# Kernel tuning notes

Hardware: AMD Instinct MI355X
Metric: run time of the kernel (lower is better)

Reference implementation:

```python
import jax, jax.numpy as jnp
import numpy as np

MAX_S, MIN_S, MAX_R = 3.0, 0.5, 3.0
A = (MAX_S - MIN_S) / 2.0   # 1.25
B = (MAX_S + MIN_S) / 2.0   # 1.75
C = (MAX_R - 1.0) / 2.0     # 1.0
D = (MAX_R + 1.0) / 2.0     # 2.0

# 3x3 kernel base points, row-major: dim0 = dy, dim1 = dx, shape [2, 9]
BASE = jnp.array([[-1, -1], [-1, 0], [-1, 1], [0, -1], [0, 0], [0, 1],
                  [1, -1], [1, 0], [1, 1]], dtype=jnp.float32).T


def conv2d(x, w, b=None):
    y = jax.lax.conv_general_dilated(x, w, window_strides=(1, 1),
                                     padding=((1, 1), (1, 1)),
                                     dimension_numbers=('NCHW', 'OIHW', 'NCHW'))
    if b is not None:
        y = y + b[None, :, None, None]
    return y


def setup_inputs() -> dict:
    key = jax.random.key(0)
    ks = jax.random.split(key, 8)
    return {
        'x': jax.random.normal(ks[0], (8, 64, 128, 128), jnp.float32),
        'w_main': jax.random.normal(ks[1], (64, 64, 3, 3), jnp.float32) * 0.05,
        'w_rot': jax.random.normal(ks[2], (2, 64, 3, 3), jnp.float32) * 0.05,
        'b_rot': jax.random.normal(ks[3], (2,), jnp.float32) * 0.05,
        'w_str': jax.random.normal(ks[4], (1, 64, 3, 3), jnp.float32) * 0.05,
        'b_str': jax.random.normal(ks[5], (1,), jnp.float32) * 0.05,
        'w_whl': jax.random.normal(ks[6], (1, 64, 3, 3), jnp.float32) * 0.05,
        'b_whl': jax.random.normal(ks[7], (1,), jnp.float32) * 0.05,
    }


def reference(x, w_main, w_rot, b_rot, w_str, b_str, w_whl, b_whl):
    b, c, H, W = x.shape
    K = 9
    # --- offset generation ---
    rot = conv2d(x, w_rot, b_rot)                     # [b,2,H,W]
    sin, cos = rot[:, 0], rot[:, 1]
    norm = jnp.sqrt(sin ** 2 + cos ** 2 + 1e-6)
    sin, cos = sin / norm, cos / norm
    r = jnp.tanh(conv2d(x, w_str, b_str))[:, 0] * A + B   # [b,H,W]
    wr = jnp.tanh(conv2d(x, w_whl, b_whl))[:, 0] * C + D  # [b,H,W]
    ky, kx = BASE[0], BASE[1]                             # [9]
    kyb = ky[None, :, None, None]
    kxb = kx[None, :, None, None]
    o0 = kyb * (wr * r)[:, None]                          # [b,9,H,W]
    o1 = kxb * wr[:, None]
    sinb, cosb = sin[:, None], cos[:, None]
    dy = cosb * o0 + sinb * o1 - kyb                      # rotation then subtract base
    dx = -sinb * o0 + cosb * o1 - kxb
    # --- deformable sampling positions (stride=1, pad=1, dil=1) ---
    py = jnp.arange(H, dtype=x.dtype)[None, None, :, None] + kyb + dy  # [b,9,H,W]
    px = jnp.arange(W, dtype=x.dtype)[None, None, None, :] + kxb + dx
    y0f = jnp.floor(py); x0f = jnp.floor(px)
    ly = py - y0f; lx = px - x0f
    y0 = y0f.astype(jnp.int32); x0 = x0f.astype(jnp.int32)
    x_flat = x.reshape(b, c, H * W)

    def gather(yi, xi, wgt):
        valid = (yi >= 0) & (yi < H) & (xi >= 0) & (xi < W)
        idx = jnp.clip(yi, 0, H - 1) * W + jnp.clip(xi, 0, W - 1)
        g = jnp.take_along_axis(x_flat, idx.reshape(b, 1, -1), axis=2)
        g = g.reshape(b, c, K, H, W)
        return g * (wgt * valid)[:, None]

    val = (gather(y0, x0, (1 - ly) * (1 - lx))
           + gather(y0, x0 + 1, (1 - ly) * lx)
           + gather(y0 + 1, x0, ly * (1 - lx))
           + gather(y0 + 1, x0 + 1, ly * lx))          # [b,c,9,H,W]
    # final 3x3 conv over sampled points == contraction over (c, k)
    out = jnp.einsum('bckhw,ock->bohw', val, w_main.reshape(w_main.shape[0], c, K))
    return out
```

## Files before the change

### kernel.cpp

```cpp
#include <hip/hip_runtime.h>
#include <hip/hip_bf16.h>
#include <hip/hip_fp16.h>
#include <math.h>

#define HH 128
#define WW 128
#define HWSZ (HH*WW)
#define CH 64
#define OC 64
#define NB 8
#define RG 28
#define RPX (RG*RG)

#define XT_BYTES   (16777216u)
#define OFFS_BYTES (2097152u)

typedef _Float16 f16x8 __attribute__((ext_vector_type(8)));
typedef __attribute__((ext_vector_type(4))) float f32x4_t;

__global__ __launch_bounds__(256) void transpose_kernel(
    const float* __restrict__ x, const float* __restrict__ w_main,
    __half* __restrict__ xT, __half* __restrict__ wmT2)
{
    const int t = threadIdx.x;
    const int i = blockIdx.x;
    if (i >= 2048) {
        const int base = (i - 2048) * 4096 + t * 16;
        #pragma unroll
        for (int j = 0; j < 16; ++j) {
            const int e = base + j;
            const int k = e >> 12;
            const int r = e & 4095;
            const int o = r >> 6;
            const int c = r & 63;
            wmT2[e] = __float2half(w_main[(size_t)o * (CH * 9) + c * 9 + k]);
        }
        return;
    }
    __shared__ float tile[64][65];
    const int b = i & 7;
    const int j = i >> 3;
    const int h  = j >> 1;
    const int w0 = (j & 1) * 64;
    const float* xb = x + (size_t)b * CH * HWSZ + h * WW + w0;
    {
        const int w = t & 63, c0 = (t >> 6) * 16;
        #pragma unroll
        for (int jj = 0; jj < 16; ++jj)
            tile[c0 + jj][w] = xb[(size_t)(c0 + jj) * HWSZ + w];
    }
    __syncthreads();
    {
        const int c = t & 63, wq = t >> 6;
        __half* o = xT + ((size_t)b * HWSZ + h * WW + w0) * 64;
        #pragma unroll
        for (int jj = 0; jj < 16; ++jj) {
            const int w = wq * 16 + jj;
            o[(size_t)w * 64 + c] = __float2half(tile[c][w]);
        }
    }
}

__global__ __launch_bounds__(256) void offsets_kernel(
    const float* __restrict__ x,
    const float* __restrict__ w_rot,
    const float* __restrict__ w_str,
    const float* __restrict__ w_whl,
    float4* __restrict__ part)
{
    __shared__ float xs[8][4][WW];
    const int t  = threadIdx.x;
    const int i  = blockIdx.x;
    const int b  = i & 7;
    const int rp = (i >> 3) & 63;
    const int cg = i >> 9;
    const int h0 = rp * 2;
    const int c0 = cg * 8;
    const float* xb = x + (size_t)b * CH * HWSZ;
    #pragma unroll
    for (int jj = 0; jj < 4; ++jj) {
        const int u   = t + jj * 256;
        const int ch  = u >> 7;
        const int rem = u & 127;
        const int row = rem >> 5;
        const int w4  = (rem & 31) * 4;
        const int grow = h0 - 1 + row;
        float4 v = make_float4(0.f, 0.f, 0.f, 0.f);
        if (grow >= 0 && grow < HH)
            v = *(const float4*)&xb[((size_t)(c0 + ch) * HH + grow) * WW + w4];
        *(float4*)&xs[ch][row][w4] = v;
    }
    __syncthreads();
    const int r = t >> 7, w = t & 127;
    const int wl = max(w - 1, 0), wr2 = min(w + 1, WW - 1);
    const float ml = (w > 0) ? 1.f : 0.f, mr = (w < WW - 1) ? 1.f : 0.f;
    float a0 = 0.f, a1 = 0.f, a2 = 0.f, a3 = 0.f;
    #pragma unroll
    for (int ch = 0; ch < 8; ++ch) {
        const int cc = c0 + ch;
        #pragma unroll
        for (int dy = 0; dy < 3; ++dy) {
            const float* row_ = &xs[ch][r + dy][0];
            const float nl = row_[wl] * ml;
            const float nc = row_[w];
            const float nr = row_[wr2] * mr;
            const int d0 = cc * 9 + dy * 3;
            a0 = fmaf(nl, w_rot[d0 + 0], a0); a0 = fmaf(nc, w_rot[d0 + 1], a0); a0 = fmaf(nr, w_rot[d0 + 2], a0);
            a1 = fmaf(nl, w_rot[576 + d0 + 0], a1); a1 = fmaf(nc, w_rot[576 + d0 + 1], a1); a1 = fmaf(nr, w_rot[576 + d0 + 2], a1);
            a2 = fmaf(nl, w_str[d0 + 0], a2); a2 = fmaf(nc, w_str[d0 + 1], a2); a2 = fmaf(nr, w_str[d0 + 2], a2);
            a3 = fmaf(nl, w_whl[d0 + 0], a3); a3 = fmaf(nc, w_whl[d0 + 1], a3); a3 = fmaf(nr, w_whl[d0 + 2], a3);
        }
    }
    part[((size_t)cg * NB + b) * HWSZ + (h0 + r) * WW + w] = make_float4(a0, a1, a2, a3);
}

__global__ __launch_bounds__(256) void reduce_kernel(
    const float4* __restrict__ part,
    const float* __restrict__ b_rot, const float* __restrict__ b_str,
    const float* __restrict__ b_whl, float4* __restrict__ offs)
{
    const int i = blockIdx.x * 256 + threadIdx.x;
    float4 s = make_float4(0.f, 0.f, 0.f, 0.f);
    #pragma unroll
    for (int cg = 0; cg < 8; ++cg) {
        const float4 p = part[(size_t)cg * NB * HWSZ + i];
        s.x += p.x; s.y += p.y; s.z += p.z; s.w += p.w;
    }
    float sv = s.x + b_rot[0], cv = s.y + b_rot[1];
    const float inv = 1.0f / sqrtf(sv * sv + cv * cv + 1e-6f);
    const float rr = tanhf(s.z + b_str[0]) * 1.25f + 1.75f;
    const float wq = tanhf(s.w + b_whl[0]) * 1.0f + 2.0f;
    offs[i] = make_float4(sv * inv, cv * inv, wq * rr, wq);
}

__global__ __launch_bounds__(256, 3) void deform_kernel(
    const __half* __restrict__ xT, const __half* __restrict__ wmT2,
    const float4* __restrict__ offs, float* __restrict__ out)
{
    __shared__ union {
        uint4 xs[RPX * 4];
        float ots[64][67];
    } sh;
    const int t  = threadIdx.x;
    const int wv = t >> 6;
    const int l  = t & 63;
    const int lm = l & 15;
    const int lg = l >> 4;
    const int i  = blockIdx.x;
    const int b  = i & 7;
    const int tile = i >> 3;
    const int w0 = (tile & 15) * 8;
    const int h0 = (tile >> 4) * 8;
    const int pi = wv * 16 + lm;
    const int h = h0 + (pi >> 3);
    const int w = w0 + (pi & 7);
    const float4 o4 = offs[(size_t)b * HWSZ + h * WW + w];
    const float sv = o4.x, cv = o4.y, av = o4.z, wvl = o4.w;
    const float hh  = (float)h;
    const float wwf = (float)w;
    const __half* xb = xT + (size_t)b * HWSZ * 64;

    int ti[9], td[9];
    __half2 w2[9][4];
    #pragma unroll
    for (int k = 0; k < 9; ++k) {
        const float kyf = (float)(k / 3) - 1.f;
        const float kxf = (float)(k % 3) - 1.f;
        const float o0v = kyf * av;
        const float o1v = kxf * wvl;
        const float pyf = hh  + cv * o0v + sv * o1v;
        const float pxf = wwf - sv * o0v + cv * o1v;
        const float y0f = floorf(pyf), x0f = floorf(pxf);
        const float ly = pyf - y0f, lx = pxf - x0f;
        const int y0 = (int)y0f, x0i = (int)x0f;
        const int y1 = y0 + 1, x1 = x0i + 1;
        const bool vy0 = (y0 >= 0) && (y0 < HH);
        const bool vy1 = (y1 >= 0) && (y1 < HH);
        const bool vx0 = (x0i >= 0) && (x0i < WW);
        const bool vx1 = (x1 >= 0) && (x1 < WW);
        w2[k][0] = __float2half2_rn((1.f - ly) * (1.f - lx) * ((vy0 && vx0) ? 1.f : 0.f));
        w2[k][1] = __float2half2_rn((1.f - ly) * lx         * ((vy0 && vx1) ? 1.f : 0.f));
        w2[k][2] = __float2half2_rn(ly * (1.f - lx)         * ((vy1 && vx0) ? 1.f : 0.f));
        w2[k][3] = __float2half2_rn(ly * lx                 * ((vy1 && vx1) ? 1.f : 0.f));
        const int iy0 = min(max(y0, 0), HH - 1), iy1 = min(max(y1, 0), HH - 1);
        const int ix0 = min(max(x0i, 0), WW - 1), ix1 = min(max(x1, 0), WW - 1);
        ti[k] = (iy0 - (h0 - 10)) * RG + (ix0 - (w0 - 10));
        td[k] = (ix1 - ix0) | ((iy1 - iy0) << 1);
    }

    f32x4_t acc0 = {0.f, 0.f, 0.f, 0.f};
    f32x4_t acc1 = acc0, acc2 = acc0, acc3 = acc0;

    for (int g = 0; g < 2; ++g) {
        __syncthreads();
        for (int u = t; u < RPX * 4; u += 256) {
            const int pxu = u >> 2, q = u & 3;
            const int lr = pxu / RG;
            const int lc = pxu - lr * RG;
            const int gy = min(max(h0 - 10 + lr, 0), HH - 1);
            const int gx = min(max(w0 - 10 + lc, 0), WW - 1);
            sh.xs[pxu * 4 + (q ^ (pxu & 3))] =
                *(const uint4*)(xb + (size_t)(gy * WW + gx) * 64 + g * 32 + q * 8);
        }
        __syncthreads();
        const int cb0 = g * 32 + lg * 8;
        #pragma unroll
        for (int k = 0; k < 9; ++k) {
            const int i00 = ti[k];
            const int dxx = td[k] & 1;
            const int dyy = (td[k] >> 1) * RG;
            const int i01 = i00 + dxx;
            const int i10 = i00 + dyy;
            const int i11 = i10 + dxx;
            union Q { uint4 q; __half2 h2[4]; };
            Q q00, q01, q10, q11;
            q00.q = sh.xs[i00 * 4 + (lg ^ (i00 & 3))];
            q01.q = sh.xs[i01 * 4 + (lg ^ (i01 & 3))];
            q10.q = sh.xs[i10 * 4 + (lg ^ (i10 & 3))];
            q11.q = sh.xs[i11 * 4 + (lg ^ (i11 & 3))];
            union { __half2 h2[4]; f16x8 v; } af;
            #pragma unroll
            for (int j = 0; j < 4; ++j) {
                af.h2[j] = __hfma2(q00.h2[j], w2[k][0],
                           __hfma2(q01.h2[j], w2[k][1],
                           __hfma2(q10.h2[j], w2[k][2],
                           __hmul2(q11.h2[j], w2[k][3]))));
            }
            const __half* wp = wmT2 + ((size_t)k * 64 + lm) * 64 + cb0;
            const f16x8 bf0 = *(const f16x8*)(wp);
            const f16x8 bf1 = *(const f16x8*)(wp + 1024);
            const f16x8 bf2v = *(const f16x8*)(wp + 2048);
            const f16x8 bf3 = *(const f16x8*)(wp + 3072);
            acc0 = __builtin_amdgcn_mfma_f32_16x16x32_f16(af.v, bf0,  acc0, 0, 0, 0);
            acc1 = __builtin_amdgcn_mfma_f32_16x16x32_f16(af.v, bf1,  acc1, 0, 0, 0);
            acc2 = __builtin_amdgcn_mfma_f32_16x16x32_f16(af.v, bf2v, acc2, 0, 0, 0);
            acc3 = __builtin_amdgcn_mfma_f32_16x16x32_f16(af.v, bf3,  acc3, 0, 0, 0);
        }
    }
    __syncthreads();
    const int pxw = wv * 16 + lg * 4;
    #pragma unroll
    for (int rg2 = 0; rg2 < 4; ++rg2) {
        sh.ots[pxw + rg2][ 0 + lm] = acc0[rg2];
        sh.ots[pxw + rg2][16 + lm] = acc1[rg2];
        sh.ots[pxw + rg2][32 + lm] = acc2[rg2];
        sh.ots[pxw + rg2][48 + lm] = acc3[rg2];
    }
    __syncthreads();
    const int oo = t >> 2;
    const int q  = (t & 3) * 16;
    #pragma unroll
    for (int j2 = 0; j2 < 4; ++j2) {
        const int px = q + j2 * 4;
        float4 v = make_float4(sh.ots[px + 0][oo], sh.ots[px + 1][oo],
                               sh.ots[px + 2][oo], sh.ots[px + 3][oo]);
        *(float4*)&out[((size_t)b * OC + oo) * HWSZ +
                       (h0 + (px >> 3)) * WW + w0 + (px & 7)] = v;
    }
}

extern "C" void kernel_launch(void* const* d_in, const int* in_sizes, int n_in,
                              void* d_out, int out_size, void* d_ws, size_t ws_size,
                              hipStream_t stream)
{
    const float* x      = (const float*)d_in[0];
    const float* w_main = (const float*)d_in[1];
    const float* w_rot  = (const float*)d_in[2];
    const float* b_rot  = (const float*)d_in[3];
    const float* w_str  = (const float*)d_in[4];
    const float* b_str  = (const float*)d_in[5];
    const float* w_whl  = (const float*)d_in[6];
    const float* b_whl  = (const float*)d_in[7];
    float* out = (float*)d_out;

    char* ws = (char*)d_ws;
    __half*  xT   = (__half*)ws;
    float4*  offs = (float4*)(ws + XT_BYTES);
    __half*  wmT2 = (__half*)(ws + XT_BYTES + OFFS_BYTES);
    float4*  part = (float4*)d_out;

    transpose_kernel<<<dim3(2057), 256, 0, stream>>>(x, w_main, xT, wmT2);
    offsets_kernel<<<dim3(4096), 256, 0, stream>>>(x, w_rot, w_str, w_whl, part);
    reduce_kernel<<<dim3(NB * HWSZ / 256), 256, 0, stream>>>(
        part, b_rot, b_str, b_whl, offs);
    deform_kernel<<<dim3(2048), 256, 0, stream>>>(xT, wmT2, offs, out);
}
```

Baseline: 213.1 us.

## Enlarge deform tile to 16x8 and stage halo via direct global-to-LDS loads

Each deform_kernel block now covers a 16x8 pixel tile with 512 threads instead of 8x8 with 256, so the 36x28 halo region is shared by twice as many pixels. This cuts redundant staging traffic per output pixel. Staging uses global_load_lds, which writes straight into LDS and skips the register round trip, and the XOR swizzle is applied on the global-address side. The offset fetch and first stage are issued before the sampling-weight computation so the two overlap. The launch bound of (512,4) may tighten the register budget and cause spills, and the larger output staging buffer raises LDS use.

```diff
diff --git a/kernel.cpp b/kernel.cpp
--- a/kernel.cpp
+++ b/kernel.cpp
@@ -9,8 +9,14 @@
 #define CH 64
 #define OC 64
 #define NB 8
-#define RG 28
-#define RPX (RG*RG)
+
+#define TH 16
+#define TW 8
+#define RGR 36
+#define RGC 28
+#define RPX2 (RGR*RGC)
+#define NQ (RPX2*4)
+#define NCHUNK (NQ/64)
 
 #define XT_BYTES   (16777216u)
 #define OFFS_BYTES (2097152u)
@@ -133,13 +139,13 @@
     offs[i] = make_float4(sv * inv, cv * inv, wq * rr, wq);
 }
 
-__global__ __launch_bounds__(256, 3) void deform_kernel(
+__global__ __launch_bounds__(512, 4) void deform_kernel(
     const __half* __restrict__ xT, const __half* __restrict__ wmT2,
     const float4* __restrict__ offs, float* __restrict__ out)
 {
     __shared__ union {
-        uint4 xs[RPX * 4];
-        float ots[64][67];
+        uint4 xs[NQ];
+        float ots[128][67];
     } sh;
     const int t  = threadIdx.x;
     const int wv = t >> 6;
@@ -149,16 +155,38 @@
     const int i  = blockIdx.x;
     const int b  = i & 7;
     const int tile = i >> 3;
-    const int w0 = (tile & 15) * 8;
-    const int h0 = (tile >> 4) * 8;
+    const int w0 = (tile & 15) * TW;
+    const int h0 = (tile >> 4) * TH;
     const int pi = wv * 16 + lm;
     const int h = h0 + (pi >> 3);
     const int w = w0 + (pi & 7);
+    const __half* xb = xT + (size_t)b * HWSZ * 64;
+
     const float4 o4 = offs[(size_t)b * HWSZ + h * WW + w];
+
+    auto stage = [&](int g) {
+        for (int c = wv; c < NCHUNK; c += 8) {
+            const int u   = c * 64 + l;
+            const int pxu = u >> 2;
+            const int sq  = u & 3;
+            const int lr  = pxu / RGC;
+            const int lc  = pxu - lr * RGC;
+            const int gy  = min(max(h0 - 10 + lr, 0), HH - 1);
+            const int gx  = min(max(w0 - 10 + lc, 0), WW - 1);
+            const int sq2 = sq ^ (pxu & 3);
+            const __half* gp = xb + ((size_t)(gy * WW + gx) * 64 + g * 32 + sq2 * 8);
+            __builtin_amdgcn_global_load_lds(
+                (const __attribute__((address_space(1))) void*)gp,
+                (__attribute__((address_space(3))) void*)((char*)sh.xs + (size_t)c * 1024),
+                16, 0, 0);
+        }
+    };
+
+    stage(0);
+
     const float sv = o4.x, cv = o4.y, av = o4.z, wvl = o4.w;
     const float hh  = (float)h;
     const float wwf = (float)w;
-    const __half* xb = xT + (size_t)b * HWSZ * 64;
 
     int ti[9], td[9];
     __half2 w2[9][4];
@@ -184,31 +212,20 @@
         w2[k][3] = __float2half2_rn(ly * lx                 * ((vy1 && vx1) ? 1.f : 0.f));
         const int iy0 = min(max(y0, 0), HH - 1), iy1 = min(max(y1, 0), HH - 1);
         const int ix0 = min(max(x0i, 0), WW - 1), ix1 = min(max(x1, 0), WW - 1);
-        ti[k] = (iy0 - (h0 - 10)) * RG + (ix0 - (w0 - 10));
+        ti[k] = (iy0 - (h0 - 10)) * RGC + (ix0 - (w0 - 10));
         td[k] = (ix1 - ix0) | ((iy1 - iy0) << 1);
     }
 
     f32x4_t acc0 = {0.f, 0.f, 0.f, 0.f};
     f32x4_t acc1 = acc0, acc2 = acc0, acc3 = acc0;
 
-    for (int g = 0; g < 2; ++g) {
-        __syncthreads();
-        for (int u = t; u < RPX * 4; u += 256) {
-            const int pxu = u >> 2, q = u & 3;
-            const int lr = pxu / RG;
-            const int lc = pxu - lr * RG;
-            const int gy = min(max(h0 - 10 + lr, 0), HH - 1);
-            const int gx = min(max(w0 - 10 + lc, 0), WW - 1);
-            sh.xs[pxu * 4 + (q ^ (pxu & 3))] =
-                *(const uint4*)(xb + (size_t)(gy * WW + gx) * 64 + g * 32 + q * 8);
-        }
-        __syncthreads();
+    auto compute = [&](int g) {
         const int cb0 = g * 32 + lg * 8;
         #pragma unroll
         for (int k = 0; k < 9; ++k) {
             const int i00 = ti[k];
             const int dxx = td[k] & 1;
-            const int dyy = (td[k] >> 1) * RG;
+            const int dyy = (td[k] >> 1) * RGC;
             const int i01 = i00 + dxx;
             const int i10 = i00 + dyy;
             const int i11 = i10 + dxx;
@@ -236,7 +253,15 @@
             acc2 = __builtin_amdgcn_mfma_f32_16x16x32_f16(af.v, bf2v, acc2, 0, 0, 0);
             acc3 = __builtin_amdgcn_mfma_f32_16x16x32_f16(af.v, bf3,  acc3, 0, 0, 0);
         }
-    }
+    };
+
+    __syncthreads();
+    compute(0);
+    __syncthreads();
+    stage(1);
+    __syncthreads();
+    compute(1);
+
     __syncthreads();
     const int pxw = wv * 16 + lg * 4;
     #pragma unroll
@@ -247,15 +272,18 @@
         sh.ots[pxw + rg2][48 + lm] = acc3[rg2];
     }
     __syncthreads();
-    const int oo = t >> 2;
-    const int q  = (t & 3) * 16;
+    const int oo = t >> 3;
+    const int s  = t & 7;
     #pragma unroll
     for (int j2 = 0; j2 < 4; ++j2) {
-        const int px = q + j2 * 4;
-        float4 v = make_float4(sh.ots[px + 0][oo], sh.ots[px + 1][oo],
-                               sh.ots[px + 2][oo], sh.ots[px + 3][oo]);
+        const int idx  = s * 4 + j2;
+        const int r    = idx >> 1;
+        const int colh = idx & 1;
+        const int p0   = r * 8 + colh * 4;
+        float4 v = make_float4(sh.ots[p0 + 0][oo], sh.ots[p0 + 1][oo],
+                               sh.ots[p0 + 2][oo], sh.ots[p0 + 3][oo]);
         *(float4*)&out[((size_t)b * OC + oo) * HWSZ +
-                       (h0 + (px >> 3)) * WW + w0 + (px & 7)] = v;
+                       (h0 + r) * WW + w0 + colh * 4] = v;
     }
 }
 
@@ -283,5 +311,5 @@
     offsets_kernel<<<dim3(4096), 256, 0, stream>>>(x, w_rot, w_str, w_whl, part);
     reduce_kernel<<<dim3(NB * HWSZ / 256), 256, 0, stream>>>(
         part, b_rot, b_str, b_whl, offs);
-    deform_kernel<<<dim3(2048), 256, 0, stream>>>(xT, wmT2, offs, out);
-}
+    deform_kernel<<<dim3(1024), 512, 0, stream>>>(xT, wmT2, offs, out);
+}
```

Result: slower. 225.1 us (+5.6%).

## Gather deformable samples directly from global memory instead of staging LDS halo

Applied to the files above, without the earlier changes.

Removes the 28x28 LDS halo tile staged per channel half and gathers the four bilinear corner vectors straight from the fp16 channel-last input in global memory. Both channel halves are processed in one pass over the 9 taps, and occupancy is raised to 4 blocks per CU because LDS use drops to the output transpose buffer. This avoids loading a large halo (784 pixels for 64 outputs) and two barriers per half, in exchange for scattered 16-byte global loads that depend on L1/L2 hits. There is also a risk of extra load latency without LDS reuse.

```diff
diff --git a/kernel.cpp b/kernel.cpp
--- a/kernel.cpp
+++ b/kernel.cpp
@@ -9,8 +9,6 @@
 #define CH 64
 #define OC 64
 #define NB 8
-#define RG 28
-#define RPX (RG*RG)
 
 #define XT_BYTES   (16777216u)
 #define OFFS_BYTES (2097152u)
@@ -133,14 +131,11 @@
     offs[i] = make_float4(sv * inv, cv * inv, wq * rr, wq);
 }
 
-__global__ __launch_bounds__(256, 3) void deform_kernel(
+__global__ __launch_bounds__(256, 4) void deform_kernel(
     const __half* __restrict__ xT, const __half* __restrict__ wmT2,
     const float4* __restrict__ offs, float* __restrict__ out)
 {
-    __shared__ union {
-        uint4 xs[RPX * 4];
-        float ots[64][67];
-    } sh;
+    __shared__ float ots[64][67];
     const int t  = threadIdx.x;
     const int wv = t >> 6;
     const int l  = t & 63;
@@ -154,13 +149,14 @@
     const int pi = wv * 16 + lm;
     const int h = h0 + (pi >> 3);
     const int w = w0 + (pi & 7);
+    const __half* xb = xT + (size_t)b * HWSZ * 64;
+
     const float4 o4 = offs[(size_t)b * HWSZ + h * WW + w];
     const float sv = o4.x, cv = o4.y, av = o4.z, wvl = o4.w;
     const float hh  = (float)h;
     const float wwf = (float)w;
-    const __half* xb = xT + (size_t)b * HWSZ * 64;
-
-    int ti[9], td[9];
+
+    int ti_[9], td_[9];
     __half2 w2[9][4];
     #pragma unroll
     for (int k = 0; k < 9; ++k) {
@@ -184,67 +180,75 @@
         w2[k][3] = __float2half2_rn(ly * lx                 * ((vy1 && vx1) ? 1.f : 0.f));
         const int iy0 = min(max(y0, 0), HH - 1), iy1 = min(max(y1, 0), HH - 1);
         const int ix0 = min(max(x0i, 0), WW - 1), ix1 = min(max(x1, 0), WW - 1);
-        ti[k] = (iy0 - (h0 - 10)) * RG + (ix0 - (w0 - 10));
-        td[k] = (ix1 - ix0) | ((iy1 - iy0) << 1);
+        ti_[k] = iy0 * WW + ix0;
+        td_[k] = (ix1 - ix0) | ((iy1 - iy0) << 1);
     }
 
     f32x4_t acc0 = {0.f, 0.f, 0.f, 0.f};
     f32x4_t acc1 = acc0, acc2 = acc0, acc3 = acc0;
 
-    for (int g = 0; g < 2; ++g) {
-        __syncthreads();
-        for (int u = t; u < RPX * 4; u += 256) {
-            const int pxu = u >> 2, q = u & 3;
-            const int lr = pxu / RG;
-            const int lc = pxu - lr * RG;
-            const int gy = min(max(h0 - 10 + lr, 0), HH - 1);
-            const int gx = min(max(w0 - 10 + lc, 0), WW - 1);
-            sh.xs[pxu * 4 + (q ^ (pxu & 3))] =
-                *(const uint4*)(xb + (size_t)(gy * WW + gx) * 64 + g * 32 + q * 8);
-        }
-        __syncthreads();
-        const int cb0 = g * 32 + lg * 8;
-        #pragma unroll
-        for (int k = 0; k < 9; ++k) {
-            const int i00 = ti[k];
-            const int dxx = td[k] & 1;
-            const int dyy = (td[k] >> 1) * RG;
-            const int i01 = i00 + dxx;
-            const int i10 = i00 + dyy;
-            const int i11 = i10 + dxx;
-            union Q { uint4 q; __half2 h2[4]; };
-            Q q00, q01, q10, q11;
-            q00.q = sh.xs[i00 * 4 + (lg ^ (i00 & 3))];
-            q01.q = sh.xs[i01 * 4 + (lg ^ (i01 & 3))];
-            q10.q = sh.xs[i10 * 4 + (lg ^ (i10 & 3))];
-            q11.q = sh.xs[i11 * 4 + (lg ^ (i11 & 3))];
-            union { __half2 h2[4]; f16x8 v; } af;
-            #pragma unroll
-            for (int j = 0; j < 4; ++j) {
-                af.h2[j] = __hfma2(q00.h2[j], w2[k][0],
-                           __hfma2(q01.h2[j], w2[k][1],
-                           __hfma2(q10.h2[j], w2[k][2],
-                           __hmul2(q11.h2[j], w2[k][3]))));
-            }
-            const __half* wp = wmT2 + ((size_t)k * 64 + lm) * 64 + cb0;
-            const f16x8 bf0 = *(const f16x8*)(wp);
-            const f16x8 bf1 = *(const f16x8*)(wp + 1024);
-            const f16x8 bf2v = *(const f16x8*)(wp + 2048);
-            const f16x8 bf3 = *(const f16x8*)(wp + 3072);
-            acc0 = __builtin_amdgcn_mfma_f32_16x16x32_f16(af.v, bf0,  acc0, 0, 0, 0);
-            acc1 = __builtin_amdgcn_mfma_f32_16x16x32_f16(af.v, bf1,  acc1, 0, 0, 0);
-            acc2 = __builtin_amdgcn_mfma_f32_16x16x32_f16(af.v, bf2v, acc2, 0, 0, 0);
-            acc3 = __builtin_amdgcn_mfma_f32_16x16x32_f16(af.v, bf3,  acc3, 0, 0, 0);
-        }
-    }
-    __syncthreads();
+    union Q { uint4 q; __half2 h2[4]; };
+    union AF { __half2 h2[4]; f16x8 v; };
+
+    #pragma unroll
+    for (int k = 0; k < 9; ++k) {
+        const int i00 = ti_[k];
+        const int dxx = td_[k] & 1;
+        const int dyy = (td_[k] >> 1) * WW;
+        const int i01 = i00 + dxx;
+        const int i10 = i00 + dyy;
+        const int i11 = i10 + dxx;
+        const __half* p00 = xb + (size_t)i00 * 64 + lg * 8;
+        const __half* p01 = xb + (size_t)i01 * 64 + lg * 8;
+        const __half* p10 = xb + (size_t)i10 * 64 + lg * 8;
+        const __half* p11 = xb + (size_t)i11 * 64 + lg * 8;
+        Q a00, a01, a10, a11, c00, c01, c10, c11;
+        a00.q = *(const uint4*)(p00);
+        a01.q = *(const uint4*)(p01);
+        a10.q = *(const uint4*)(p10);
+        a11.q = *(const uint4*)(p11);
+        c00.q = *(const uint4*)(p00 + 32);
+        c01.q = *(const uint4*)(p01 + 32);
+        c10.q = *(const uint4*)(p10 + 32);
+        c11.q = *(const uint4*)(p11 + 32);
+        AF af0, af1;
+        #pragma unroll
+        for (int j = 0; j < 4; ++j) {
+            af0.h2[j] = __hfma2(a00.h2[j], w2[k][0],
+                        __hfma2(a01.h2[j], w2[k][1],
+                        __hfma2(a10.h2[j], w2[k][2],
+                        __hmul2(a11.h2[j], w2[k][3]))));
+            af1.h2[j] = __hfma2(c00.h2[j], w2[k][0],
+                        __hfma2(c01.h2[j], w2[k][1],
+                        __hfma2(c10.h2[j], w2[k][2],
+                        __hmul2(c11.h2[j], w2[k][3]))));
+        }
+        const __half* wp = wmT2 + ((size_t)k * 64 + lm) * 64 + lg * 8;
+        const f16x8 b00 = *(const f16x8*)(wp);
+        const f16x8 b01 = *(const f16x8*)(wp + 1024);
+        const f16x8 b02 = *(const f16x8*)(wp + 2048);
+        const f16x8 b03 = *(const f16x8*)(wp + 3072);
+        const f16x8 b10 = *(const f16x8*)(wp + 32);
+        const f16x8 b11 = *(const f16x8*)(wp + 1024 + 32);
+        const f16x8 b12 = *(const f16x8*)(wp + 2048 + 32);
+        const f16x8 b13 = *(const f16x8*)(wp + 3072 + 32);
+        acc0 = __builtin_amdgcn_mfma_f32_16x16x32_f16(af0.v, b00, acc0, 0, 0, 0);
+        acc1 = __builtin_amdgcn_mfma_f32_16x16x32_f16(af0.v, b01, acc1, 0, 0, 0);
+        acc2 = __builtin_amdgcn_mfma_f32_16x16x32_f16(af0.v, b02, acc2, 0, 0, 0);
+        acc3 = __builtin_amdgcn_mfma_f32_16x16x32_f16(af0.v, b03, acc3, 0, 0, 0);
+        acc0 = __builtin_amdgcn_mfma_f32_16x16x32_f16(af1.v, b10, acc0, 0, 0, 0);
+        acc1 = __builtin_amdgcn_mfma_f32_16x16x32_f16(af1.v, b11, acc1, 0, 0, 0);
+        acc2 = __builtin_amdgcn_mfma_f32_16x16x32_f16(af1.v, b12, acc2, 0, 0, 0);
+        acc3 = __builtin_amdgcn_mfma_f32_16x16x32_f16(af1.v, b13, acc3, 0, 0, 0);
+    }
+
     const int pxw = wv * 16 + lg * 4;
     #pragma unroll
     for (int rg2 = 0; rg2 < 4; ++rg2) {
-        sh.ots[pxw + rg2][ 0 + lm] = acc0[rg2];
-        sh.ots[pxw + rg2][16 + lm] = acc1[rg2];
-        sh.ots[pxw + rg2][32 + lm] = acc2[rg2];
-        sh.ots[pxw + rg2][48 + lm] = acc3[rg2];
+        ots[pxw + rg2][ 0 + lm] = acc0[rg2];
+        ots[pxw + rg2][16 + lm] = acc1[rg2];
+        ots[pxw + rg2][32 + lm] = acc2[rg2];
+        ots[pxw + rg2][48 + lm] = acc3[rg2];
     }
     __syncthreads();
     const int oo = t >> 2;
@@ -252,8 +256,8 @@
     #pragma unroll
     for (int j2 = 0; j2 < 4; ++j2) {
         const int px = q + j2 * 4;
-        float4 v = make_float4(sh.ots[px + 0][oo], sh.ots[px + 1][oo],
-                               sh.ots[px + 2][oo], sh.ots[px + 3][oo]);
+        float4 v = make_float4(ots[px + 0][oo], ots[px + 1][oo],
+                               ots[px + 2][oo], ots[px + 3][oo]);
         *(float4*)&out[((size_t)b * OC + oo) * HWSZ +
                        (h0 + (px >> 3)) * WW + w0 + (px & 7)] = v;
     }
```

New measurement: 252.4 us. 1.18x slower.

## Merge transpose and offset kernels; prefetch tiles and weights in deform kernel

Applied to the files above, without the earlier changes.

Fuses the transpose and offsets kernels into one launch so they can run concurrently on the GPU. In the deform kernel, the first channel-half tile is loaded into registers before the offset and bilinear index math, so global-load latency overlaps with that computation. The next tap's weight fragments are prefetched during the current tap's MFMAs, and shared-memory indices are precomputed with a changed swizzle. In exchange, the extra staged uint4 registers (13 of them) may reduce occupancy.

```diff
diff --git a/kernel.cpp b/kernel.cpp
--- a/kernel.cpp
+++ b/kernel.cpp
@@ -18,14 +18,19 @@
 typedef _Float16 f16x8 __attribute__((ext_vector_type(8)));
 typedef __attribute__((ext_vector_type(4))) float f32x4_t;
 
-__global__ __launch_bounds__(256) void transpose_kernel(
+__global__ __launch_bounds__(256) void pre_kernel(
     const float* __restrict__ x, const float* __restrict__ w_main,
-    __half* __restrict__ xT, __half* __restrict__ wmT2)
+    const float* __restrict__ w_rot, const float* __restrict__ w_str,
+    const float* __restrict__ w_whl,
+    __half* __restrict__ xT, __half* __restrict__ wmT2,
+    float4* __restrict__ part)
 {
+    __shared__ float shmem[64 * 65];
     const int t = threadIdx.x;
     const int i = blockIdx.x;
-    if (i >= 2048) {
-        const int base = (i - 2048) * 4096 + t * 16;
+
+    if (i >= 6144) {
+        const int base = (i - 6144) * 4096 + t * 16;
         #pragma unroll
         for (int j = 0; j < 16; ++j) {
             const int e = base + j;
@@ -37,40 +42,35 @@
         }
         return;
     }
-    __shared__ float tile[64][65];
-    const int b = i & 7;
-    const int j = i >> 3;
-    const int h  = j >> 1;
-    const int w0 = (j & 1) * 64;
-    const float* xb = x + (size_t)b * CH * HWSZ + h * WW + w0;
-    {
-        const int w = t & 63, c0 = (t >> 6) * 16;
-        #pragma unroll
-        for (int jj = 0; jj < 16; ++jj)
-            tile[c0 + jj][w] = xb[(size_t)(c0 + jj) * HWSZ + w];
-    }
-    __syncthreads();
-    {
-        const int c = t & 63, wq = t >> 6;
-        __half* o = xT + ((size_t)b * HWSZ + h * WW + w0) * 64;
-        #pragma unroll
-        for (int jj = 0; jj < 16; ++jj) {
-            const int w = wq * 16 + jj;
-            o[(size_t)w * 64 + c] = __float2half(tile[c][w]);
-        }
-    }
-}
-
-__global__ __launch_bounds__(256) void offsets_kernel(
-    const float* __restrict__ x,
-    const float* __restrict__ w_rot,
-    const float* __restrict__ w_str,
-    const float* __restrict__ w_whl,
-    float4* __restrict__ part)
-{
-    __shared__ float xs[8][4][WW];
-    const int t  = threadIdx.x;
-    const int i  = blockIdx.x;
+
+    if (i >= 4096) {
+        float (*tile)[65] = (float(*)[65])shmem;
+        const int it = i - 4096;
+        const int b = it & 7;
+        const int j = it >> 3;
+        const int h  = j >> 1;
+        const int w0 = (j & 1) * 64;
+        const float* xb = x + (size_t)b * CH * HWSZ + h * WW + w0;
+        {
+            const int w = t & 63, c0 = (t >> 6) * 16;
+            #pragma unroll
+            for (int jj = 0; jj < 16; ++jj)
+                tile[c0 + jj][w] = xb[(size_t)(c0 + jj) * HWSZ + w];
+        }
+        __syncthreads();
+        {
+            const int c = t & 63, wq = t >> 6;
+            __half* o = xT + ((size_t)b * HWSZ + h * WW + w0) * 64;
+            #pragma unroll
+            for (int jj = 0; jj < 16; ++jj) {
+                const int w = wq * 16 + jj;
+                o[(size_t)w * 64 + c] = __float2half(tile[c][w]);
+            }
+        }
+        return;
+    }
+
+    float (*xs)[4][WW] = (float(*)[4][WW])shmem;
     const int b  = i & 7;
     const int rp = (i >> 3) & 63;
     const int cg = i >> 9;
@@ -154,13 +154,28 @@
     const int pi = wv * 16 + lm;
     const int h = h0 + (pi >> 3);
     const int w = w0 + (pi & 7);
+    const __half* xb = xT + (size_t)b * HWSZ * 64;
+
+    uint4 st[13];
+    #pragma unroll
+    for (int j = 0; j < 13; ++j) {
+        const int u = t + j * 256;
+        if (u < RPX * 4) {
+            const int pxu = u >> 2, q = u & 3;
+            const int lr = pxu / RG;
+            const int lc = pxu - lr * RG;
+            const int gy = min(max(h0 - 10 + lr, 0), HH - 1);
+            const int gx = min(max(w0 - 10 + lc, 0), WW - 1);
+            st[j] = *(const uint4*)(xb + (size_t)(gy * WW + gx) * 64 + q * 8);
+        }
+    }
+
     const float4 o4 = offs[(size_t)b * HWSZ + h * WW + w];
     const float sv = o4.x, cv = o4.y, av = o4.z, wvl = o4.w;
     const float hh  = (float)h;
     const float wwf = (float)w;
-    const __half* xb = xT + (size_t)b * HWSZ * 64;
-
-    int ti[9], td[9];
+
+    int idx00[9], idx01[9], idx10[9], idx11[9];
     __half2 w2[9][4];
     #pragma unroll
     for (int k = 0; k < 9; ++k) {
@@ -184,59 +199,82 @@
         w2[k][3] = __float2half2_rn(ly * lx                 * ((vy1 && vx1) ? 1.f : 0.f));
         const int iy0 = min(max(y0, 0), HH - 1), iy1 = min(max(y1, 0), HH - 1);
         const int ix0 = min(max(x0i, 0), WW - 1), ix1 = min(max(x1, 0), WW - 1);
-        ti[k] = (iy0 - (h0 - 10)) * RG + (ix0 - (w0 - 10));
-        td[k] = (ix1 - ix0) | ((iy1 - iy0) << 1);
+        const int dyy = iy1 - iy0, dxx = ix1 - ix0;
+        const int p00 = (iy0 - (h0 - 10)) * RG + (ix0 - (w0 - 10));
+        const int p01 = p00 + dxx;
+        const int p10 = p00 + dyy * RG;
+        const int p11 = p10 + dxx;
+        idx00[k] = p00 * 4 + (lg ^ ((p00 >> 1) & 3));
+        idx01[k] = p01 * 4 + (lg ^ ((p01 >> 1) & 3));
+        idx10[k] = p10 * 4 + (lg ^ ((p10 >> 1) & 3));
+        idx11[k] = p11 * 4 + (lg ^ ((p11 >> 1) & 3));
+    }
+
+    #pragma unroll
+    for (int j = 0; j < 13; ++j) {
+        const int u = t + j * 256;
+        if (u < RPX * 4) {
+            const int pxu = u >> 2, q = u & 3;
+            sh.xs[pxu * 4 + (q ^ ((pxu >> 1) & 3))] = st[j];
+        }
     }
 
     f32x4_t acc0 = {0.f, 0.f, 0.f, 0.f};
     f32x4_t acc1 = acc0, acc2 = acc0, acc3 = acc0;
 
-    for (int g = 0; g < 2; ++g) {
-        __syncthreads();
-        for (int u = t; u < RPX * 4; u += 256) {
-            const int pxu = u >> 2, q = u & 3;
-            const int lr = pxu / RG;
-            const int lc = pxu - lr * RG;
-            const int gy = min(max(h0 - 10 + lr, 0), HH - 1);
-            const int gx = min(max(w0 - 10 + lc, 0), WW - 1);
-            sh.xs[pxu * 4 + (q ^ (pxu & 3))] =
-                *(const uint4*)(xb + (size_t)(gy * WW + gx) * 64 + g * 32 + q * 8);
-        }
-        __syncthreads();
+    auto compute = [&](int g) {
         const int cb0 = g * 32 + lg * 8;
+        const __half* wb = wmT2 + lm * 64 + cb0;
+        f16x8 bc0 = *(const f16x8*)(wb);
+        f16x8 bc1 = *(const f16x8*)(wb + 1024);
+        f16x8 bc2 = *(const f16x8*)(wb + 2048);
+        f16x8 bc3 = *(const f16x8*)(wb + 3072);
         #pragma unroll
         for (int k = 0; k < 9; ++k) {
-            const int i00 = ti[k];
-            const int dxx = td[k] & 1;
-            const int dyy = (td[k] >> 1) * RG;
-            const int i01 = i00 + dxx;
-            const int i10 = i00 + dyy;
-            const int i11 = i10 + dxx;
+            f16x8 bn0, bn1, bn2, bn3;
+            if (k < 8) {
+                const __half* wp = wb + (size_t)(k + 1) * 4096;
+                bn0 = *(const f16x8*)(wp);
+                bn1 = *(const f16x8*)(wp + 1024);
+                bn2 = *(const f16x8*)(wp + 2048);
+                bn3 = *(const f16x8*)(wp + 3072);
+            }
             union Q { uint4 q; __half2 h2[4]; };
             Q q00, q01, q10, q11;
-            q00.q = sh.xs[i00 * 4 + (lg ^ (i00 & 3))];
-            q01.q = sh.xs[i01 * 4 + (lg ^ (i01 & 3))];
-            q10.q = sh.xs[i10 * 4 + (lg ^ (i10 & 3))];
-            q11.q = sh.xs[i11 * 4 + (lg ^ (i11 & 3))];
+            q00.q = sh.xs[idx00[k]];
+            q01.q = sh.xs[idx01[k]];
+            q10.q = sh.xs[idx10[k]];
+            q11.q = sh.xs[idx11[k]];
             union { __half2 h2[4]; f16x8 v; } af;
             #pragma unroll
             for (int j = 0; j < 4; ++j) {
-                af.h2[j] = __hfma2(q00.h2[j], w2[k][0],
-                           __hfma2(q01.h2[j], w2[k][1],
-                           __hfma2(q10.h2[j], w2[k][2],
-                           __hmul2(q11.h2[j], w2[k][3]))));
+                const __half2 e0 = __hfma2(q00.h2[j], w2[k][0], __hmul2(q01.h2[j], w2[k][1]));
+                const __half2 e1 = __hfma2(q10.h2[j], w2[k][2], __hmul2(q11.h2[j], w2[k][3]));
+                af.h2[j] = __hadd2(e0, e1);
             }
-            const __half* wp = wmT2 + ((size_t)k * 64 + lm) * 64 + cb0;
-            const f16x8 bf0 = *(const f16x8*)(wp);
-            const f16x8 bf1 = *(const f16x8*)(wp + 1024);
-            const f16x8 bf2v = *(const f16x8*)(wp + 2048);
-            const f16x8 bf3 = *(const f16x8*)(wp + 3072);
-            acc0 = __builtin_amdgcn_mfma_f32_16x16x32_f16(af.v, bf0,  acc0, 0, 0, 0);
-            acc1 = __builtin_amdgcn_mfma_f32_16x16x32_f16(af.v, bf1,  acc1, 0, 0, 0);
-            acc2 = __builtin_amdgcn_mfma_f32_16x16x32_f16(af.v, bf2v, acc2, 0, 0, 0);
-            acc3 = __builtin_amdgcn_mfma_f32_16x16x32_f16(af.v, bf3,  acc3, 0, 0, 0);
-        }
-    }
+            acc0 = __builtin_amdgcn_mfma_f32_16x16x32_f16(af.v, bc0, acc0, 0, 0, 0);
+            acc1 = __builtin_amdgcn_mfma_f32_16x16x32_f16(af.v, bc1, acc1, 0, 0, 0);
+            acc2 = __builtin_amdgcn_mfma_f32_16x16x32_f16(af.v, bc2, acc2, 0, 0, 0);
+            acc3 = __builtin_amdgcn_mfma_f32_16x16x32_f16(af.v, bc3, acc3, 0, 0, 0);
+            if (k < 8) { bc0 = bn0; bc1 = bn1; bc2 = bn2; bc3 = bn3; }
+        }
+    };
+
+    __syncthreads();
+    compute(0);
+    __syncthreads();
+    for (int u = t; u < RPX * 4; u += 256) {
+        const int pxu = u >> 2, q = u & 3;
+        const int lr = pxu / RG;
+        const int lc = pxu - lr * RG;
+        const int gy = min(max(h0 - 10 + lr, 0), HH - 1);
+        const int gx = min(max(w0 - 10 + lc, 0), WW - 1);
+        sh.xs[pxu * 4 + (q ^ ((pxu >> 1) & 3))] =
+            *(const uint4*)(xb + (size_t)(gy * WW + gx) * 64 + 32 + q * 8);
+    }
+    __syncthreads();
+    compute(1);
+
     __syncthreads();
     const int pxw = wv * 16 + lg * 4;
     #pragma unroll
@@ -279,8 +317,8 @@
     __half*  wmT2 = (__half*)(ws + XT_BYTES + OFFS_BYTES);
     float4*  part = (float4*)d_out;
 
-    transpose_kernel<<<dim3(2057), 256, 0, stream>>>(x, w_main, xT, wmT2);
-    offsets_kernel<<<dim3(4096), 256, 0, stream>>>(x, w_rot, w_str, w_whl, part);
+    pre_kernel<<<dim3(6153), 256, 0, stream>>>(x, w_main, w_rot, w_str, w_whl,
+                                               xT, wmT2, part);
     reduce_kernel<<<dim3(NB * HWSZ / 256), 256, 0, stream>>>(
         part, b_rot, b_str, b_whl, offs);
     deform_kernel<<<dim3(2048), 256, 0, stream>>>(xT, wmT2, offs, out);
```

After: 263.6 us. 23.7% more time.
